# Kernel tuning notes

Measured on AMD Instinct MI355X. Metric: run time of the kernel, lower is better.

The kernel has to match this reference:

```python
import jax, jax.numpy as jnp
import numpy as np

BLOCK_SIZE = 16
MODEL_CONTEXT_LEN = 4096
NUM_KV_HEADS = 8
HEAD_DIM = 128
ROPE_BASE = 10000.0


def _rope(x, pos):
    """Neox-style rotary embedding. x: [B, T, H, D], pos: [T] int."""
    D = x.shape[-1]
    inv_freq = 1.0 / (ROPE_BASE ** (jnp.arange(0, D // 2, dtype=jnp.float32) * 2.0 / D))
    f = pos.astype(jnp.float32)[:, None] * inv_freq  # [T, D/2]
    cos = jnp.cos(f)[None, :, None, :]
    sin = jnp.sin(f)[None, :, None, :]
    x1, x2 = jnp.split(x, 2, axis=-1)
    return jnp.concatenate([x1 * cos - x2 * sin, x2 * cos + x1 * sin], axis=-1)


def setup_inputs() -> dict:
    key = jax.random.key(0)
    k1, k2, k3, k4, k5 = jax.random.split(key, 5)
    B = 8
    HD = NUM_KV_HEADS * HEAD_DIM
    blocks_per_seq = 256
    num_blocks = B * blocks_per_seq
    return {
        "q": jax.random.normal(k1, (B, HD), dtype=jnp.float32),
        "k": jax.random.normal(k2, (B, HD), dtype=jnp.float32),
        "v": jax.random.normal(k3, (B, HD), dtype=jnp.float32),
        "key_cache": jax.random.normal(k4, (num_blocks, BLOCK_SIZE, NUM_KV_HEADS, HEAD_DIM), dtype=jnp.float32),
        "value_cache": jax.random.normal(k5, (num_blocks, BLOCK_SIZE, NUM_KV_HEADS, HEAD_DIM), dtype=jnp.float32),
        "block_tables": jnp.arange(B * blocks_per_seq, dtype=jnp.int32).reshape(B, blocks_per_seq),
        "positions": jnp.zeros((B,), dtype=jnp.int32),
        "seq_len": 8192,
    }


def reference(q, k, v, key_cache, value_cache, block_tables, positions, seq_len):
    # Decode step of StreamingAttentionSink (_forward_rope, FLASH_ATTN layout),
    # seq_len > model_context_len => streaming sink branch. Cache restoration
    # side-effects are identities on the output, so only attention is computed.
    B = q.shape[0]
    H, D, bs = NUM_KV_HEADS, HEAD_DIM, BLOCK_SIZE
    q = q.reshape(B, H, D)
    k = k.reshape(B, H, D)
    v = v.reshape(B, H, D)

    num_past_tokens = seq_len - 1              # real past length (static python int)
    rem = num_past_tokens % bs                 # tokens in the last (partial) block

    # Gather past K/V from paged cache: full blocks + remainder of last block.
    full_k = key_cache[block_tables[:, :-1]].reshape(B, -1, H, D)   # [B, 255*bs, H, D]
    full_v = value_cache[block_tables[:, :-1]].reshape(B, -1, H, D)
    rem_k = key_cache[block_tables[:, -1], :rem]                    # [B, rem, H, D]
    rem_v = value_cache[block_tables[:, -1], :rem]
    past_k = jnp.concatenate([full_k, rem_k], axis=1)               # [B, P, H, D]
    past_v = jnp.concatenate([full_v, rem_v], axis=1)
    P = past_k.shape[1]                                             # = ctx - bs + rem

    # Re-apply RoPE: sink block keeps positions [0, bs); recent keys get
    # positions [2*bs-1-rem, ctx-1) -> concatenated this is contiguous 0..P-1.
    pos_past = jnp.arange(P, dtype=jnp.int32)
    past_k = _rope(past_k, pos_past)

    # Query (and current key) at capped position model_context_len - 1.
    pos_q = jnp.array([MODEL_CONTEXT_LEN - 1], dtype=jnp.int32)
    q_r = _rope(q[:, None], pos_q)[:, 0]        # [B, H, D]
    k_r = _rope(k[:, None], pos_q)              # [B, 1, H, D]

    keys = jnp.concatenate([past_k, k_r], axis=1)           # [B, P+1, H, D]
    vals = jnp.concatenate([past_v, v[:, None]], axis=1)

    scale = 1.0 / jnp.sqrt(jnp.float32(D))
    scores = jnp.einsum('bhd,bkhd->bhk', q_r, keys) * scale  # [B, H, P+1]
    probs = jax.nn.softmax(scores, axis=-1)
    out = jnp.einsum('bhk,bkhd->bhd', probs, vals)           # [B, H, D]
    return out.reshape(B, H * D)
```

## Files before the change

### kernel.cpp

```cpp
#include <hip/hip_runtime.h>
#include <math.h>

#define NUM_KV_HEADS 8
#define HEAD_DIM 128
#define HD (NUM_KV_HEADS * HEAD_DIM)
#define BLOCK_SZ 16
#define MODEL_CTX 4096
#define CHUNK 128
#define BLKS_PER_CHUNK (CHUNK / BLOCK_SZ)

__global__ void rope_table(float* __restrict__ tab, int ntab) {
    const int idx = blockIdx.x * 256 + threadIdx.x;
    if (idx >= ntab * 64) return;
    const int t = idx >> 6;
    const int f = idx & 63;
    const float inv = expf(-9.210340371976184f * (float)f * (1.0f / 64.0f));
    float s, c;
    sincosf((float)t * inv, &s, &c);
    tab[2 * idx]     = c;
    tab[2 * idx + 1] = s;
}

__global__ __launch_bounds__(256, 8)
void attn_partial(const float* __restrict__ q,
                  const float* __restrict__ knew,
                  const float* __restrict__ vnew,
                  const float* __restrict__ kcache,
                  const float* __restrict__ vcache,
                  const int* __restrict__ btab,
                  const int* __restrict__ seqlen_p,
                  const float* __restrict__ tab,
                  int nbps,
                  float* __restrict__ o_part,
                  float* __restrict__ m_part,
                  float* __restrict__ l_part,
                  int n_chunks)
{
    const int chunk = blockIdx.x;
    const int bh    = blockIdx.y;
    const int b     = bh / NUM_KV_HEADS;
    const int h     = bh % NUM_KV_HEADS;
    const int tid   = threadIdx.x;
    const int lane  = tid & 63;
    const int wave  = tid >> 6;
    const int sl    = lane & 31;
    const int half  = lane >> 5;
    const int hw    = wave * 2 + half;

    __shared__ float sc[CHUNK];
    __shared__ float red[8];
    __shared__ int   sblk[BLKS_PER_CHUNK];
    __shared__ float po[8][HEAD_DIM];

    const int seq_len = *seqlen_p;
    const int rem = (seq_len - 1) & (BLOCK_SZ - 1);
    const int T   = (nbps - 1) * BLOCK_SZ + rem + 1;

    if (tid < BLKS_PER_CHUNK)
        sblk[tid] = btab[b * nbps + chunk * BLKS_PER_CHUNK + tid];
    __syncthreads();

    const float* qb = q + (size_t)b * HD + h * HEAD_DIM;
    const float2 qa  = *(const float2*)(qb + 2 * sl);
    const float2 qb2 = *(const float2*)(qb + 64 + 2 * sl);
    const float4 qcs = *(const float4*)(tab + (size_t)(MODEL_CTX - 1) * 128 + 4 * sl);
    const float qr1a = qa.x * qcs.x - qb2.x * qcs.y;
    const float qr1b = qa.y * qcs.z - qb2.y * qcs.w;
    const float qr2a = qb2.x * qcs.x + qa.x * qcs.y;
    const float qr2b = qb2.y * qcs.z + qa.y * qcs.w;

    const int t0 = chunk * CHUNK;
    const size_t head_off = (size_t)h * HEAD_DIM;
    const float scale = 0.08838834764831845f;

    const int blk = sblk[hw];
    const float* kbase = kcache + (size_t)blk * BLOCK_SZ * HD + head_off;
    const float* vbase = vcache + (size_t)blk * BLOCK_SZ * HD + head_off;
    const float* knb = knew + (size_t)b * HD + head_off;
    const float* vnb = vnew + (size_t)b * HD + head_off;
    const int tbase = t0 + hw * BLOCK_SZ;

    for (int j4 = 0; j4 < BLOCK_SZ; j4 += 4) {
        float2 ka[4], kb2v[4];
        float4 cs[4];
        int    valid[4];
        #pragma unroll
        for (int u = 0; u < 4; u++) {
            const int j = j4 + u;
            const int t = tbase + j;
            const bool newlike = (t >= T - 1);
            const float* kp = newlike ? knb : (kbase + (size_t)j * HD);
            const int tt = newlike ? (MODEL_CTX - 1) : t;
            ka[u]   = *(const float2*)(kp + 2 * sl);
            kb2v[u] = *(const float2*)(kp + 64 + 2 * sl);
            cs[u]   = *(const float4*)(tab + (size_t)tt * 128 + 4 * sl);
            valid[u] = (t < T);
        }
        #pragma unroll
        for (int u = 0; u < 4; u++) {
            const float r1a = ka[u].x  * cs[u].x - kb2v[u].x * cs[u].y;
            const float r1b = ka[u].y  * cs[u].z - kb2v[u].y * cs[u].w;
            const float r2a = kb2v[u].x * cs[u].x + ka[u].x  * cs[u].y;
            const float r2b = kb2v[u].y * cs[u].z + ka[u].y  * cs[u].w;
            float d = r1a * qr1a + r1b * qr1b + r2a * qr2a + r2b * qr2b;
            #pragma unroll
            for (int off = 1; off < 32; off <<= 1) d += __shfl_xor(d, off, 64);
            const float score = valid[u] ? d * scale : -INFINITY;
            if (sl == 0) sc[j4 + u + hw * BLOCK_SZ] = score;
        }
    }
    __syncthreads();

    float sv = 0.0f;
    if (wave < 2) {
        sv = sc[tid];
        float mloc = sv;
        #pragma unroll
        for (int off = 1; off < 64; off <<= 1) mloc = fmaxf(mloc, __shfl_xor(mloc, off, 64));
        if (lane == 0) red[wave] = mloc;
    }
    __syncthreads();
    const float m = fmaxf(red[0], red[1]);
    if (wave < 2) {
        const float p = __expf(sv - m);
        sc[tid] = p;
        float ls = p;
        #pragma unroll
        for (int off = 1; off < 64; off <<= 1) ls += __shfl_xor(ls, off, 64);
        if (lane == 0) red[4 + wave] = ls;
    }
    __syncthreads();
    const float l = red[4] + red[5];

    float a1a = 0.f, a1b = 0.f, a2a = 0.f, a2b = 0.f;
    for (int j4 = 0; j4 < BLOCK_SZ; j4 += 4) {
        float2 va[4], vb2v[4];
        float  pw[4];
        #pragma unroll
        for (int u = 0; u < 4; u++) {
            const int j = j4 + u;
            const int t = tbase + j;
            const float* vp = (t >= T - 1) ? vnb : (vbase + (size_t)j * HD);
            va[u]   = *(const float2*)(vp + 2 * sl);
            vb2v[u] = *(const float2*)(vp + 64 + 2 * sl);
            pw[u]   = sc[hw * BLOCK_SZ + j];
        }
        #pragma unroll
        for (int u = 0; u < 4; u++) {
            a1a += pw[u] * va[u].x;
            a1b += pw[u] * va[u].y;
            a2a += pw[u] * vb2v[u].x;
            a2b += pw[u] * vb2v[u].y;
        }
    }
    po[hw][2 * sl]      = a1a;
    po[hw][2 * sl + 1]  = a1b;
    po[hw][64 + 2 * sl] = a2a;
    po[hw][65 + 2 * sl] = a2b;
    __syncthreads();

    if (tid < HEAD_DIM) {
        float s = 0.f;
        #pragma unroll
        for (int j = 0; j < 8; j++) s += po[j][tid];
        o_part[((size_t)bh * n_chunks + chunk) * HEAD_DIM + tid] = s;
    }
    if (tid == 0) {
        m_part[bh * n_chunks + chunk] = m;
        l_part[bh * n_chunks + chunk] = l;
    }
}

__global__ void attn_combine(const float* __restrict__ o_part,
                             const float* __restrict__ m_part,
                             const float* __restrict__ l_part,
                             float* __restrict__ out,
                             int n_chunks)
{
    const int bh = blockIdx.x;
    const int d  = threadIdx.x;

    float M = -INFINITY;
    for (int c = 0; c < n_chunks; c++) M = fmaxf(M, m_part[bh * n_chunks + c]);
    float L = 0.f, num = 0.f;
    for (int c = 0; c < n_chunks; c++) {
        const float w = __expf(m_part[bh * n_chunks + c] - M);
        L   += l_part[bh * n_chunks + c] * w;
        num += w * o_part[((size_t)bh * n_chunks + c) * HEAD_DIM + d];
    }
    out[(size_t)bh * HEAD_DIM + d] = num / L;
}

extern "C" void kernel_launch(void* const* d_in, const int* in_sizes, int n_in,
                              void* d_out, int out_size, void* d_ws, size_t ws_size,
                              hipStream_t stream) {
    const float* q  = (const float*)d_in[0];
    const float* k  = (const float*)d_in[1];
    const float* v  = (const float*)d_in[2];
    const float* kc = (const float*)d_in[3];
    const float* vc = (const float*)d_in[4];
    const int* bt   = (const int*)d_in[5];
    const int* slp  = (const int*)d_in[7];

    const int B    = in_sizes[0] / HD;
    const int nbps = in_sizes[5] / B;
    const int n_chunks = (nbps * BLOCK_SZ + CHUNK - 1) / CHUNK;
    const int BH = B * NUM_KV_HEADS;

    int ntab = nbps * BLOCK_SZ;
    if (ntab < MODEL_CTX) ntab = MODEL_CTX;

    float* tab    = (float*)d_ws;
    float* o_part = tab + (size_t)ntab * 128;
    float* m_part = o_part + (size_t)BH * n_chunks * HEAD_DIM;
    float* l_part = m_part + (size_t)BH * n_chunks;

    const int ttotal = ntab * 64;
    rope_table<<<(ttotal + 255) / 256, 256, 0, stream>>>(tab, ntab);

    dim3 g1(n_chunks, BH);
    attn_partial<<<g1, 256, 0, stream>>>(q, k, v, kc, vc, bt, slp, tab, nbps,
                                         o_part, m_part, l_part, n_chunks);
    attn_combine<<<dim3(BH), HEAD_DIM, 0, stream>>>(o_part, m_part, l_part,
                                                    (float*)d_out, n_chunks);
}
```

Before: 303.0 us.

## Rewrite attention partial kernel with per-wave online softmax and batched K/V loads

Restructures the per-chunk attention kernel so each 16-lane group handles one token with float4 loads, and K, V and RoPE table loads for two tokens are issued together. Softmax becomes an online running max/sum per lane group, merged across groups with shuffles and across waves through a small shared buffer. This removes the separate score, softmax and PV phases and several block-wide barriers, and overlaps V loads with K loads. It lowers the occupancy hint from 8 to 6 to give room for the higher register use, and adds extra exp work per token.

After: 332.2 us. +9.6%, slower.

```diff
diff --git a/kernel.cpp b/kernel.cpp
--- a/kernel.cpp
+++ b/kernel.cpp
@@ -21,7 +21,7 @@
     tab[2 * idx + 1] = s;
 }
 
-__global__ __launch_bounds__(256, 8)
+__global__ __launch_bounds__(256, 6)
 void attn_partial(const float* __restrict__ q,
                   const float* __restrict__ knew,
                   const float* __restrict__ vnew,
@@ -43,131 +43,149 @@
     const int tid   = threadIdx.x;
     const int lane  = tid & 63;
     const int wave  = tid >> 6;
-    const int sl    = lane & 31;
-    const int half  = lane >> 5;
-    const int hw    = wave * 2 + half;
-
-    __shared__ float sc[CHUNK];
-    __shared__ float red[8];
-    __shared__ int   sblk[BLKS_PER_CHUNK];
-    __shared__ float po[8][HEAD_DIM];
+    const int g     = lane >> 4;
+    const int m16   = lane & 15;
+
+    __shared__ __align__(16) float wo[4][HEAD_DIM];
+    __shared__ float wm[4], wl[4];
 
     const int seq_len = *seqlen_p;
     const int rem = (seq_len - 1) & (BLOCK_SZ - 1);
     const int T   = (nbps - 1) * BLOCK_SZ + rem + 1;
 
-    if (tid < BLKS_PER_CHUNK)
-        sblk[tid] = btab[b * nbps + chunk * BLKS_PER_CHUNK + tid];
-    __syncthreads();
-
     const float* qb = q + (size_t)b * HD + h * HEAD_DIM;
-    const float2 qa  = *(const float2*)(qb + 2 * sl);
-    const float2 qb2 = *(const float2*)(qb + 64 + 2 * sl);
-    const float4 qcs = *(const float4*)(tab + (size_t)(MODEL_CTX - 1) * 128 + 4 * sl);
-    const float qr1a = qa.x * qcs.x - qb2.x * qcs.y;
-    const float qr1b = qa.y * qcs.z - qb2.y * qcs.w;
-    const float qr2a = qb2.x * qcs.x + qa.x * qcs.y;
-    const float qr2b = qb2.y * qcs.z + qa.y * qcs.w;
+    const float4 q1  = *(const float4*)(qb + 4 * m16);
+    const float4 q2  = *(const float4*)(qb + 64 + 4 * m16);
+    const float4 tq1 = *(const float4*)(tab + (size_t)(MODEL_CTX - 1) * 128 + 8 * m16);
+    const float4 tq2 = *(const float4*)(tab + (size_t)(MODEL_CTX - 1) * 128 + 8 * m16 + 4);
+    float4 qr1, qr2;
+    qr1.x = q1.x * tq1.x - q2.x * tq1.y;  qr2.x = q2.x * tq1.x + q1.x * tq1.y;
+    qr1.y = q1.y * tq1.z - q2.y * tq1.w;  qr2.y = q2.y * tq1.z + q1.y * tq1.w;
+    qr1.z = q1.z * tq2.x - q2.z * tq2.y;  qr2.z = q2.z * tq2.x + q1.z * tq2.y;
+    qr1.w = q1.w * tq2.z - q2.w * tq2.w;  qr2.w = q2.w * tq2.z + q1.w * tq2.w;
 
     const int t0 = chunk * CHUNK;
     const size_t head_off = (size_t)h * HEAD_DIM;
     const float scale = 0.08838834764831845f;
 
-    const int blk = sblk[hw];
-    const float* kbase = kcache + (size_t)blk * BLOCK_SZ * HD + head_off;
-    const float* vbase = vcache + (size_t)blk * BLOCK_SZ * HD + head_off;
+    const int bti  = b * nbps + chunk * BLKS_PER_CHUNK;
+    const int blk0 = btab[bti + wave * 2];
+    const int blk1 = btab[bti + wave * 2 + 1];
+    const float* kb0 = kcache + (size_t)blk0 * BLOCK_SZ * HD + head_off;
+    const float* kb1 = kcache + (size_t)blk1 * BLOCK_SZ * HD + head_off;
+    const float* vb0 = vcache + (size_t)blk0 * BLOCK_SZ * HD + head_off;
+    const float* vb1 = vcache + (size_t)blk1 * BLOCK_SZ * HD + head_off;
     const float* knb = knew + (size_t)b * HD + head_off;
     const float* vnb = vnew + (size_t)b * HD + head_off;
-    const int tbase = t0 + hw * BLOCK_SZ;
-
-    for (int j4 = 0; j4 < BLOCK_SZ; j4 += 4) {
-        float2 ka[4], kb2v[4];
-        float4 cs[4];
-        int    valid[4];
+
+    float4 o1 = {0.f, 0.f, 0.f, 0.f};
+    float4 o2 = {0.f, 0.f, 0.f, 0.f};
+    float mrun = -1e30f, lrun = 0.f;
+
+    const int tw = t0 + wave * 32;
+
+    #pragma unroll
+    for (int jj = 0; jj < 4; jj++) {
+        const int locA = (2 * jj) * 4 + g;
+        const int locB = (2 * jj + 1) * 4 + g;
+        const int tA = tw + locA;
+        const int tB = tw + locB;
+        const bool nlA = (tA >= T - 1);
+        const bool nlB = (tB >= T - 1);
+        const float* kpA = nlA ? knb : ((locA < 16 ? kb0 : kb1) + (size_t)(locA & 15) * HD);
+        const float* vpA = nlA ? vnb : ((locA < 16 ? vb0 : vb1) + (size_t)(locA & 15) * HD);
+        const float* kpB = nlB ? knb : ((locB < 16 ? kb0 : kb1) + (size_t)(locB & 15) * HD);
+        const float* vpB = nlB ? vnb : ((locB < 16 ? vb0 : vb1) + (size_t)(locB & 15) * HD);
+        const int ttA = nlA ? (MODEL_CTX - 1) : tA;
+        const int ttB = nlB ? (MODEL_CTX - 1) : tB;
+
+        const float4 kA1 = *(const float4*)(kpA + 4 * m16);
+        const float4 kA2 = *(const float4*)(kpA + 64 + 4 * m16);
+        const float4 kB1 = *(const float4*)(kpB + 4 * m16);
+        const float4 kB2 = *(const float4*)(kpB + 64 + 4 * m16);
+        const float4 vA1 = *(const float4*)(vpA + 4 * m16);
+        const float4 vA2 = *(const float4*)(vpA + 64 + 4 * m16);
+        const float4 vB1 = *(const float4*)(vpB + 4 * m16);
+        const float4 vB2 = *(const float4*)(vpB + 64 + 4 * m16);
+        const float4 cA1 = *(const float4*)(tab + (size_t)ttA * 128 + 8 * m16);
+        const float4 cA2 = *(const float4*)(tab + (size_t)ttA * 128 + 8 * m16 + 4);
+        const float4 cB1 = *(const float4*)(tab + (size_t)ttB * 128 + 8 * m16);
+        const float4 cB2 = *(const float4*)(tab + (size_t)ttB * 128 + 8 * m16 + 4);
+
+        float dA =
+            (kA1.x * cA1.x - kA2.x * cA1.y) * qr1.x + (kA2.x * cA1.x + kA1.x * cA1.y) * qr2.x
+          + (kA1.y * cA1.z - kA2.y * cA1.w) * qr1.y + (kA2.y * cA1.z + kA1.y * cA1.w) * qr2.y
+          + (kA1.z * cA2.x - kA2.z * cA2.y) * qr1.z + (kA2.z * cA2.x + kA1.z * cA2.y) * qr2.z
+          + (kA1.w * cA2.z - kA2.w * cA2.w) * qr1.w + (kA2.w * cA2.z + kA1.w * cA2.w) * qr2.w;
+        float dB =
+            (kB1.x * cB1.x - kB2.x * cB1.y) * qr1.x + (kB2.x * cB1.x + kB1.x * cB1.y) * qr2.x
+          + (kB1.y * cB1.z - kB2.y * cB1.w) * qr1.y + (kB2.y * cB1.z + kB1.y * cB1.w) * qr2.y
+          + (kB1.z * cB2.x - kB2.z * cB2.y) * qr1.z + (kB2.z * cB2.x + kB1.z * cB2.y) * qr2.z
+          + (kB1.w * cB2.z - kB2.w * cB2.w) * qr1.w + (kB2.w * cB2.z + kB1.w * cB2.w) * qr2.w;
+
         #pragma unroll
-        for (int u = 0; u < 4; u++) {
-            const int j = j4 + u;
-            const int t = tbase + j;
-            const bool newlike = (t >= T - 1);
-            const float* kp = newlike ? knb : (kbase + (size_t)j * HD);
-            const int tt = newlike ? (MODEL_CTX - 1) : t;
-            ka[u]   = *(const float2*)(kp + 2 * sl);
-            kb2v[u] = *(const float2*)(kp + 64 + 2 * sl);
-            cs[u]   = *(const float4*)(tab + (size_t)tt * 128 + 4 * sl);
-            valid[u] = (t < T);
+        for (int off = 1; off < 16; off <<= 1) {
+            dA += __shfl_xor(dA, off, 64);
+            dB += __shfl_xor(dB, off, 64);
         }
-        #pragma unroll
-        for (int u = 0; u < 4; u++) {
-            const float r1a = ka[u].x  * cs[u].x - kb2v[u].x * cs[u].y;
-            const float r1b = ka[u].y  * cs[u].z - kb2v[u].y * cs[u].w;
-            const float r2a = kb2v[u].x * cs[u].x + ka[u].x  * cs[u].y;
-            const float r2b = kb2v[u].y * cs[u].z + ka[u].y  * cs[u].w;
-            float d = r1a * qr1a + r1b * qr1b + r2a * qr2a + r2b * qr2b;
-            #pragma unroll
-            for (int off = 1; off < 32; off <<= 1) d += __shfl_xor(d, off, 64);
-            const float score = valid[u] ? d * scale : -INFINITY;
-            if (sl == 0) sc[j4 + u + hw * BLOCK_SZ] = score;
+
+        const float sA = (tA < T) ? dA * scale : -INFINITY;
+        const float sB = (tB < T) ? dB * scale : -INFINITY;
+
+        const float mnew = fmaxf(mrun, fmaxf(sA, sB));
+        const float c  = __expf(mrun - mnew);
+        const float pA = __expf(sA - mnew);
+        const float pB = __expf(sB - mnew);
+        mrun = mnew;
+        lrun = lrun * c + pA + pB;
+        o1.x = o1.x * c + pA * vA1.x + pB * vB1.x;
+        o1.y = o1.y * c + pA * vA1.y + pB * vB1.y;
+        o1.z = o1.z * c + pA * vA1.z + pB * vB1.z;
+        o1.w = o1.w * c + pA * vA1.w + pB * vB1.w;
+        o2.x = o2.x * c + pA * vA2.x + pB * vB2.x;
+        o2.y = o2.y * c + pA * vA2.y + pB * vB2.y;
+        o2.z = o2.z * c + pA * vA2.z + pB * vB2.z;
+        o2.w = o2.w * c + pA * vA2.w + pB * vB2.w;
+    }
+
+    float mo = fmaxf(mrun, __shfl_xor(mrun, 16, 64));
+    mo = fmaxf(mo, __shfl_xor(mo, 32, 64));
+    const float w = __expf(mrun - mo);
+    float lw = lrun * w;
+    o1.x *= w; o1.y *= w; o1.z *= w; o1.w *= w;
+    o2.x *= w; o2.y *= w; o2.z *= w; o2.w *= w;
+    #pragma unroll
+    for (int off = 16; off < 64; off <<= 1) {
+        lw   += __shfl_xor(lw, off, 64);
+        o1.x += __shfl_xor(o1.x, off, 64);
+        o1.y += __shfl_xor(o1.y, off, 64);
+        o1.z += __shfl_xor(o1.z, off, 64);
+        o1.w += __shfl_xor(o1.w, off, 64);
+        o2.x += __shfl_xor(o2.x, off, 64);
+        o2.y += __shfl_xor(o2.y, off, 64);
+        o2.z += __shfl_xor(o2.z, off, 64);
+        o2.w += __shfl_xor(o2.w, off, 64);
+    }
+
+    if (g == 0) {
+        *(float4*)&wo[wave][4 * m16]      = o1;
+        *(float4*)&wo[wave][64 + 4 * m16] = o2;
+        if (m16 == 0) { wm[wave] = mo; wl[wave] = lw; }
+    }
+    __syncthreads();
+
+    if (tid < HEAD_DIM) {
+        const float m0 = wm[0], m1 = wm[1], m2 = wm[2], m3 = wm[3];
+        const float M = fmaxf(fmaxf(m0, m1), fmaxf(m2, m3));
+        const float w0 = __expf(m0 - M), w1 = __expf(m1 - M);
+        const float w2 = __expf(m2 - M), w3 = __expf(m3 - M);
+        const float num = w0 * wo[0][tid] + w1 * wo[1][tid]
+                        + w2 * wo[2][tid] + w3 * wo[3][tid];
+        o_part[((size_t)bh * n_chunks + chunk) * HEAD_DIM + tid] = num;
+        if (tid == 0) {
+            m_part[bh * n_chunks + chunk] = M;
+            l_part[bh * n_chunks + chunk] = w0 * wl[0] + w1 * wl[1] + w2 * wl[2] + w3 * wl[3];
         }
-    }
-    __syncthreads();
-
-    float sv = 0.0f;
-    if (wave < 2) {
-        sv = sc[tid];
-        float mloc = sv;
-        #pragma unroll
-        for (int off = 1; off < 64; off <<= 1) mloc = fmaxf(mloc, __shfl_xor(mloc, off, 64));
-        if (lane == 0) red[wave] = mloc;
-    }
-    __syncthreads();
-    const float m = fmaxf(red[0], red[1]);
-    if (wave < 2) {
-        const float p = __expf(sv - m);
-        sc[tid] = p;
-        float ls = p;
-        #pragma unroll
-        for (int off = 1; off < 64; off <<= 1) ls += __shfl_xor(ls, off, 64);
-        if (lane == 0) red[4 + wave] = ls;
-    }
-    __syncthreads();
-    const float l = red[4] + red[5];
-
-    float a1a = 0.f, a1b = 0.f, a2a = 0.f, a2b = 0.f;
-    for (int j4 = 0; j4 < BLOCK_SZ; j4 += 4) {
-        float2 va[4], vb2v[4];
-        float  pw[4];
-        #pragma unroll
-        for (int u = 0; u < 4; u++) {
-            const int j = j4 + u;
-            const int t = tbase + j;
-            const float* vp = (t >= T - 1) ? vnb : (vbase + (size_t)j * HD);
-            va[u]   = *(const float2*)(vp + 2 * sl);
-            vb2v[u] = *(const float2*)(vp + 64 + 2 * sl);
-            pw[u]   = sc[hw * BLOCK_SZ + j];
-        }
-        #pragma unroll
-        for (int u = 0; u < 4; u++) {
-            a1a += pw[u] * va[u].x;
-            a1b += pw[u] * va[u].y;
-            a2a += pw[u] * vb2v[u].x;
-            a2b += pw[u] * vb2v[u].y;
-        }
-    }
-    po[hw][2 * sl]      = a1a;
-    po[hw][2 * sl + 1]  = a1b;
-    po[hw][64 + 2 * sl] = a2a;
-    po[hw][65 + 2 * sl] = a2b;
-    __syncthreads();
-
-    if (tid < HEAD_DIM) {
-        float s = 0.f;
-        #pragma unroll
-        for (int j = 0; j < 8; j++) s += po[j][tid];
-        o_part[((size_t)bh * n_chunks + chunk) * HEAD_DIM + tid] = s;
-    }
-    if (tid == 0) {
-        m_part[bh * n_chunks + chunk] = m;
-        l_part[bh * n_chunks + chunk] = l;
     }
 }
 
```
